# Performance work log

Measured on AMD Instinct MI355X. Metric: run time of the kernel, lower is better.

The kernel has to match this reference:

```python
import jax, jax.numpy as jnp
import numpy as np

NEG_INF = -1.0e9  # matches module's negativeInfinity buffer


def setup_inputs() -> dict:
    key = jax.random.key(0)
    k0, k1, k2, k3 = jax.random.split(key, 4)
    bs, h, dh, qsl, sl = 2048, 8, 32, 64, 64
    q = jax.random.normal(k0, (bs, h, dh, qsl, 1), dtype=jnp.float32)
    k = jax.random.normal(k1, (bs, h, dh, 1, sl), dtype=jnp.float32)
    v = jax.random.normal(k2, (bs, h, dh, sl), dtype=jnp.float32)
    mask = jnp.zeros((bs, 1, qsl, sl), dtype=bool)
    gamma = jnp.ones((h,), dtype=jnp.float32)   # qk_GBN gamma
    bias = jax.random.normal(k3, (h,), dtype=jnp.float32) * 0.01  # qk_GBN bias
    return {"q": q, "k": k, "v": v, "mask": mask, "gamma": gamma, "bias": bias}


def reference(q, k, v, mask, gamma, bias):
    # scores: elementwise q*k summed over head-dim -> [bs, h, qsl, sl]
    qk = (q * k).sum(axis=2)
    # qk_GBN eval path: running m=0, s=1 -> per-head affine
    qk = qk * gamma[None, :, None, None] + bias[None, :, None, None]
    qk = jnp.where(mask, NEG_INF, qk)
    v_weights = jax.nn.softmax(qk, axis=-1)
    v_weights = jnp.where(mask, 0.0, v_weights)
    # sigmoid gating of attention weights
    v_weights = v_weights * jax.nn.sigmoid(qk)
    # output = v @ v_weights^T -> [bs, h, dvh, qsl]
    out = jnp.einsum("bhds,bhqs->bhdq", v, v_weights)
    return out
```

## Files before the change

### kernel.cpp

```cpp
#include <hip/hip_runtime.h>

typedef __attribute__((ext_vector_type(4))) float  f32x4;
typedef __attribute__((ext_vector_type(8))) __bf16 bf16x8;
typedef __attribute__((ext_vector_type(4))) __bf16 bf16x4;

#define MFMA16(a, b, c) __builtin_amdgcn_mfma_f32_16x16x32_bf16((a), (b), (c), 0, 0, 0)

__global__ __launch_bounds__(256, 8)
void mha_fused(const float* __restrict__ qg, const float* __restrict__ kg,
               const float* __restrict__ vg, const unsigned char* __restrict__ maskg,
               const float* __restrict__ gammag, const float* __restrict__ biasg,
               float* __restrict__ outg)
{
    const int bid = blockIdx.x;
    const int chunk = gridDim.x >> 3;
    const int bh = (bid & 7) * chunk + (bid >> 3);
    const int b  = bh >> 3;
    const int h  = bh & 7;
    const int t  = threadIdx.x;

    __shared__ __bf16 sKh[64][40];
    __shared__ __bf16 sKl[64][40];
    __shared__ __bf16 sV [32][72];

    const float* qb = qg + (size_t)bh * 2048;
    const float* kb = kg + (size_t)bh * 2048;
    const float* vb = vg + (size_t)bh * 2048;
    const unsigned char* mb = maskg + (size_t)b * 4096;
    float* ob = outg + (size_t)bh * 2048;

    const int w  = t >> 6;
    const int li = t & 15;
    const int hi = (t >> 4) & 3;
    const int i  = w * 16 + li;

    float qv[8];
    #pragma unroll
    for (int e = 0; e < 8; ++e) qv[e] = qb[(hi * 8 + e) * 64 + i];
    unsigned int mw[4];
    #pragma unroll
    for (int jt = 0; jt < 4; ++jt)
        mw[jt] = *(const unsigned int*)&mb[i * 64 + jt * 16 + hi * 4];

    {
        const int j = t & 63, sel = t >> 6;
        float a[8];
        #pragma unroll
        for (int e = 0; e < 8; ++e) a[e] = kb[(sel * 8 + e) * 64 + j];
        bf16x8 h8, l8;
        #pragma unroll
        for (int e = 0; e < 8; ++e) {
            __bf16 hh = (__bf16)a[e];
            h8[e] = hh;
            l8[e] = (__bf16)(a[e] - (float)hh);
        }
        const int slot = sel ^ ((j >> 3) & 3);
        *(bf16x8*)&sKh[j][slot * 8] = h8;
        *(bf16x8*)&sKl[j][slot * 8] = l8;
    }
    {
        const int d = t >> 3, j0 = (t & 7) * 8;
        f32x4 x0 = *(const f32x4*)&vb[d * 64 + j0];
        f32x4 x1 = *(const f32x4*)&vb[d * 64 + j0 + 4];
        bf16x8 vv = {(__bf16)x0[0], (__bf16)x0[1], (__bf16)x0[2], (__bf16)x0[3],
                     (__bf16)x1[0], (__bf16)x1[1], (__bf16)x1[2], (__bf16)x1[3]};
        *(bf16x8*)&sV[d][j0] = vv;
    }

    bf16x8 qh, ql;
    #pragma unroll
    for (int e = 0; e < 8; ++e) {
        __bf16 hh = (__bf16)qv[e];
        qh[e] = hh;
        ql[e] = (__bf16)(qv[e] - (float)hh);
    }

    __syncthreads();

    const float ga = gammag[h], be = biasg[h];
    float s[16];
    #pragma unroll
    for (int jt = 0; jt < 4; ++jt) {
        const int j = jt * 16 + li;
        const int slot = hi ^ ((j >> 3) & 3);
        bf16x8 ah = *(bf16x8*)&sKh[j][slot * 8];
        bf16x8 al = *(bf16x8*)&sKl[j][slot * 8];
        f32x4 c = {0.f, 0.f, 0.f, 0.f};
        c = MFMA16(al, qh, c);
        c = MFMA16(ah, ql, c);
        c = MFMA16(ah, qh, c);
        #pragma unroll
        for (int r = 0; r < 4; ++r) {
            float x = c[r] * ga + be;
            if ((mw[jt] >> (8 * r)) & 0xffu) x = -1.0e9f;
            s[jt * 4 + r] = x;
        }
    }

    float m = s[0];
    #pragma unroll
    for (int e = 1; e < 16; ++e) m = fmaxf(m, s[e]);
    m = fmaxf(m, __shfl_xor(m, 16));
    m = fmaxf(m, __shfl_xor(m, 32));
    float p[16], sum = 0.f;
    #pragma unroll
    for (int e = 0; e < 16; ++e) { p[e] = __expf(s[e] - m); sum += p[e]; }
    sum += __shfl_xor(sum, 16);
    sum += __shfl_xor(sum, 32);
    const float inv = 1.0f / sum;

    bf16x4 wv[4];
    #pragma unroll
    for (int jt = 0; jt < 4; ++jt) {
        #pragma unroll
        for (int r = 0; r < 4; ++r) {
            const int e = jt * 4 + r;
            const float g = 1.0f / (1.0f + __expf(-s[e]));
            wv[jt][r] = (__bf16)(p[e] * inv * g);
        }
    }

    f32x4 o0 = {0.f, 0.f, 0.f, 0.f};
    f32x4 o1 = {0.f, 0.f, 0.f, 0.f};
    #pragma unroll
    for (int kt = 0; kt < 2; ++kt) {
        bf16x4 wlo = wv[2 * kt], whi = wv[2 * kt + 1];
        bf16x8 wb = {wlo[0], wlo[1], wlo[2], wlo[3], whi[0], whi[1], whi[2], whi[3]};
        const int c0 = kt * 32 + hi * 4;
        const int c1 = kt * 32 + 16 + hi * 4;
        bf16x4 a0l = *(const bf16x4*)&sV[li][c0];
        bf16x4 a0h = *(const bf16x4*)&sV[li][c1];
        bf16x8 va = {a0l[0], a0l[1], a0l[2], a0l[3], a0h[0], a0h[1], a0h[2], a0h[3]};
        bf16x4 a1l = *(const bf16x4*)&sV[16 + li][c0];
        bf16x4 a1h = *(const bf16x4*)&sV[16 + li][c1];
        bf16x8 vc = {a1l[0], a1l[1], a1l[2], a1l[3], a1h[0], a1h[1], a1h[2], a1h[3]};
        o0 = MFMA16(va, wb, o0);
        o1 = MFMA16(vc, wb, o1);
    }
    #pragma unroll
    for (int r = 0; r < 4; ++r) {
        ob[(hi * 4 + r) * 64 + i]      = o0[r];
        ob[(16 + hi * 4 + r) * 64 + i] = o1[r];
    }
}

extern "C" void kernel_launch(void* const* d_in, const int* in_sizes, int n_in,
                              void* d_out, int out_size, void* d_ws, size_t ws_size,
                              hipStream_t stream)
{
    const float* q = (const float*)d_in[0];
    const float* k = (const float*)d_in[1];
    const float* v = (const float*)d_in[2];
    const unsigned char* mask = (const unsigned char*)d_in[3];
    const float* gamma = (const float*)d_in[4];
    const float* bias  = (const float*)d_in[5];
    float* out = (float*)d_out;

    const int num_bh = in_sizes[0] / 2048;
    dim3 grid(num_bh), block(256);
    hipLaunchKernelGGL(mha_fused, grid, block, 0, stream,
                       q, k, v, mask, gamma, bias, out);
}
```

Measured before the change: 110.0 us.

## Reuse softmax exponent for sigmoid, hoist global loads, drop block swizzle

Computes the sigmoid gate from the already computed softmax exponent, using sigmoid(s) = p/(p+exp(-m)), which removes a second exp per element. All global loads (K, V, Q, mask) are issued up front behind a sched_barrier so their latency overlaps. The grid-index swizzle is removed and the occupancy hint is lowered from 8 to 4 blocks per CU. The algebraic identity can lose precision when exp(-m) overflows or underflows, and lower occupancy may reduce latency hiding.

Result: faster. 105.0 us (-4.5%).

```diff
diff --git a/kernel.cpp b/kernel.cpp
--- a/kernel.cpp
+++ b/kernel.cpp
@@ -6,15 +6,13 @@
 
 #define MFMA16(a, b, c) __builtin_amdgcn_mfma_f32_16x16x32_bf16((a), (b), (c), 0, 0, 0)
 
-__global__ __launch_bounds__(256, 8)
+__global__ __launch_bounds__(256, 4)
 void mha_fused(const float* __restrict__ qg, const float* __restrict__ kg,
                const float* __restrict__ vg, const unsigned char* __restrict__ maskg,
                const float* __restrict__ gammag, const float* __restrict__ biasg,
                float* __restrict__ outg)
 {
-    const int bid = blockIdx.x;
-    const int chunk = gridDim.x >> 3;
-    const int bh = (bid & 7) * chunk + (bid >> 3);
+    const int bh = blockIdx.x;
     const int b  = bh >> 3;
     const int h  = bh & 7;
     const int t  = threadIdx.x;
@@ -26,7 +24,7 @@
     const float* qb = qg + (size_t)bh * 2048;
     const float* kb = kg + (size_t)bh * 2048;
     const float* vb = vg + (size_t)bh * 2048;
-    const unsigned char* mb = maskg + (size_t)b * 4096;
+    const unsigned char* mbp = maskg + (size_t)b * 4096;
     float* ob = outg + (size_t)bh * 2048;
 
     const int w  = t >> 6;
@@ -34,47 +32,46 @@
     const int hi = (t >> 4) & 3;
     const int i  = w * 16 + li;
 
+    const int jK  = t & 63, sel = t >> 6;
+    float a[8];
+    #pragma unroll
+    for (int e = 0; e < 8; ++e) a[e] = kb[(sel * 8 + e) * 64 + jK];
+    f32x4 x0 = *(const f32x4*)(vb + t * 8);
+    f32x4 x1 = *(const f32x4*)(vb + t * 8 + 4);
     float qv[8];
     #pragma unroll
     for (int e = 0; e < 8; ++e) qv[e] = qb[(hi * 8 + e) * 64 + i];
     unsigned int mw[4];
     #pragma unroll
     for (int jt = 0; jt < 4; ++jt)
-        mw[jt] = *(const unsigned int*)&mb[i * 64 + jt * 16 + hi * 4];
+        mw[jt] = *(const unsigned int*)&mbp[i * 64 + jt * 16 + hi * 4];
+    __builtin_amdgcn_sched_barrier(0);
 
     {
-        const int j = t & 63, sel = t >> 6;
-        float a[8];
-        #pragma unroll
-        for (int e = 0; e < 8; ++e) a[e] = kb[(sel * 8 + e) * 64 + j];
         bf16x8 h8, l8;
         #pragma unroll
         for (int e = 0; e < 8; ++e) {
-            __bf16 hh = (__bf16)a[e];
+            const __bf16 hh = (__bf16)a[e];
             h8[e] = hh;
             l8[e] = (__bf16)(a[e] - (float)hh);
         }
-        const int slot = sel ^ ((j >> 3) & 3);
-        *(bf16x8*)&sKh[j][slot * 8] = h8;
-        *(bf16x8*)&sKl[j][slot * 8] = l8;
+        const int slot = sel ^ ((jK >> 3) & 3);
+        *(bf16x8*)&sKh[jK][slot * 8] = h8;
+        *(bf16x8*)&sKl[jK][slot * 8] = l8;
     }
     {
         const int d = t >> 3, j0 = (t & 7) * 8;
-        f32x4 x0 = *(const f32x4*)&vb[d * 64 + j0];
-        f32x4 x1 = *(const f32x4*)&vb[d * 64 + j0 + 4];
         bf16x8 vv = {(__bf16)x0[0], (__bf16)x0[1], (__bf16)x0[2], (__bf16)x0[3],
                      (__bf16)x1[0], (__bf16)x1[1], (__bf16)x1[2], (__bf16)x1[3]};
         *(bf16x8*)&sV[d][j0] = vv;
     }
-
     bf16x8 qh, ql;
     #pragma unroll
     for (int e = 0; e < 8; ++e) {
-        __bf16 hh = (__bf16)qv[e];
+        const __bf16 hh = (__bf16)qv[e];
         qh[e] = hh;
         ql[e] = (__bf16)(qv[e] - (float)hh);
     }
-
     __syncthreads();
 
     const float ga = gammag[h], be = biasg[h];
@@ -102,9 +99,10 @@
     for (int e = 1; e < 16; ++e) m = fmaxf(m, s[e]);
     m = fmaxf(m, __shfl_xor(m, 16));
     m = fmaxf(m, __shfl_xor(m, 32));
-    float p[16], sum = 0.f;
+    const float em = __expf(-m);
+    float sum = 0.f;
     #pragma unroll
-    for (int e = 0; e < 16; ++e) { p[e] = __expf(s[e] - m); sum += p[e]; }
+    for (int e = 0; e < 16; ++e) { s[e] = __expf(s[e] - m); sum += s[e]; }
     sum += __shfl_xor(sum, 16);
     sum += __shfl_xor(sum, 32);
     const float inv = 1.0f / sum;
@@ -114,9 +112,8 @@
     for (int jt = 0; jt < 4; ++jt) {
         #pragma unroll
         for (int r = 0; r < 4; ++r) {
-            const int e = jt * 4 + r;
-            const float g = 1.0f / (1.0f + __expf(-s[e]));
-            wv[jt][r] = (__bf16)(p[e] * inv * g);
+            const float p = s[jt * 4 + r];
+            wv[jt][r] = (__bf16)(p * inv * __fdividef(p, p + em));
         }
     }
 
@@ -124,8 +121,8 @@
     f32x4 o1 = {0.f, 0.f, 0.f, 0.f};
     #pragma unroll
     for (int kt = 0; kt < 2; ++kt) {
-        bf16x4 wlo = wv[2 * kt], whi = wv[2 * kt + 1];
-        bf16x8 wb = {wlo[0], wlo[1], wlo[2], wlo[3], whi[0], whi[1], whi[2], whi[3]};
+        bf16x4 wlo = wv[2 * kt], whi2 = wv[2 * kt + 1];
+        bf16x8 wb = {wlo[0], wlo[1], wlo[2], wlo[3], whi2[0], whi2[1], whi2[2], whi2[3]};
         const int c0 = kt * 32 + hi * 4;
         const int c1 = kt * 32 + 16 + hi * 4;
         bf16x4 a0l = *(const bf16x4*)&sV[li][c0];
```
